# Kernel tuning notes

Hardware: AMD Instinct MI355X
Metric: run time of the kernel (lower is better)

Reference implementation:

```python
import jax, jax.numpy as jnp
import numpy as np

L = 6      # layers (enc and dec)
D = 512    # d_model
H = 8      # heads
DK = D // H
F = 2048   # dim_feedforward
B = 8
S = 512    # src len
T = 512    # tgt len
NEG = -1e9


def setup_inputs() -> dict:
    key = jax.random.key(0)
    ks = jax.random.split(key, 64)
    it = iter(ks)
    def w(shape, scale=0.02):
        return jax.random.normal(next(it), shape, dtype=jnp.float32) * scale
    inp = {}
    inp['src'] = jax.random.normal(next(it), (B, S, D), dtype=jnp.float32)
    inp['tgt'] = jax.random.normal(next(it), (B, T, D), dtype=jnp.float32)
    inp['tgt_mask'] = jnp.where(jnp.triu(jnp.ones((T, T), bool), 1), jnp.float32(NEG), jnp.float32(0.0))
    # encoder params (stacked over L layers)
    inp['enc_Wq'] = w((L, H, D, DK)); inp['enc_Wk'] = w((L, H, D, DK)); inp['enc_Wv'] = w((L, H, D, DK))
    inp['enc_Wo'] = w((L, D, D))
    inp['enc_ln1_a'] = jnp.ones((L, D)); inp['enc_ln1_b'] = jnp.zeros((L, D))
    inp['enc_W1'] = w((L, D, F)); inp['enc_b1'] = jnp.zeros((L, F))
    inp['enc_W2'] = w((L, F, D)); inp['enc_b2'] = jnp.zeros((L, D))
    inp['enc_ln2_a'] = jnp.ones((L, D)); inp['enc_ln2_b'] = jnp.zeros((L, D))
    # decoder params
    inp['dec_sWq'] = w((L, H, D, DK)); inp['dec_sWk'] = w((L, H, D, DK)); inp['dec_sWv'] = w((L, H, D, DK))
    inp['dec_sWo'] = w((L, D, D))
    inp['dec_ln1_a'] = jnp.ones((L, D)); inp['dec_ln1_b'] = jnp.zeros((L, D))
    inp['dec_cWq'] = w((L, H, D, DK)); inp['dec_cWk'] = w((L, H, D, DK)); inp['dec_cWv'] = w((L, H, D, DK))
    inp['dec_cWo'] = w((L, D, D))
    inp['dec_ln2_a'] = jnp.ones((L, D)); inp['dec_ln2_b'] = jnp.zeros((L, D))
    inp['dec_W1'] = w((L, D, F)); inp['dec_b1'] = jnp.zeros((L, F))
    inp['dec_W2'] = w((L, F, D)); inp['dec_b2'] = jnp.zeros((L, D))
    inp['dec_ln3_a'] = jnp.ones((L, D)); inp['dec_ln3_b'] = jnp.zeros((L, D))
    return inp


def layernorm(x, a, b):
    # faithful to the torch module: unbiased std (ddof=1) and eps added to std
    mean = x.mean(-1, keepdims=True)
    std = jnp.std(x, axis=-1, keepdims=True, ddof=1)
    return a * (x - mean) / (std + 1e-6) + b


def mha(qx, kx, vx, Wq, Wk, Wv, Wo, mask):
    # Wq/Wk/Wv: [H, D, dk] (per-head torch loop fused into one batched einsum)
    q = jnp.einsum('bsd,hdk->bhsk', qx, Wq)
    k = jnp.einsum('bsd,hdk->bhsk', kx, Wk)
    v = jnp.einsum('bsd,hdk->bhsk', vx, Wv)
    scores = jnp.einsum('bhqk,bhmk->bhqm', q, k) / np.float32(np.sqrt(Wq.shape[-1]))
    if mask is not None:
        scores = scores + mask  # [T,T] broadcasts over batch and heads
    attn = jax.nn.softmax(scores, axis=-1)
    o = jnp.einsum('bhqm,bhmk->bhqk', attn, v)
    b_, h_, s_, k_ = o.shape
    o = o.transpose(0, 2, 1, 3).reshape(b_, s_, h_ * k_)  # concat heads
    return o @ Wo


def ffn(x, W1, b1, W2, b2):
    return jnp.maximum(x @ W1 + b1, 0.0) @ W2 + b2


def reference(src, tgt, tgt_mask,
              enc_Wq, enc_Wk, enc_Wv, enc_Wo, enc_ln1_a, enc_ln1_b,
              enc_W1, enc_b1, enc_W2, enc_b2, enc_ln2_a, enc_ln2_b,
              dec_sWq, dec_sWk, dec_sWv, dec_sWo, dec_ln1_a, dec_ln1_b,
              dec_cWq, dec_cWk, dec_cWv, dec_cWo, dec_ln2_a, dec_ln2_b,
              dec_W1, dec_b1, dec_W2, dec_b2, dec_ln3_a, dec_ln3_b):
    # encoder
    x = src
    for i in range(L):
        h = x + mha(x, x, x, enc_Wq[i], enc_Wk[i], enc_Wv[i], enc_Wo[i], None)
        x = layernorm(h, enc_ln1_a[i], enc_ln1_b[i])
        h = x + ffn(x, enc_W1[i], enc_b1[i], enc_W2[i], enc_b2[i])
        x = layernorm(h, enc_ln2_a[i], enc_ln2_b[i])
    memory = x
    # decoder
    y = tgt
    for i in range(L):
        h = y + mha(y, y, y, dec_sWq[i], dec_sWk[i], dec_sWv[i], dec_sWo[i], tgt_mask)
        y = layernorm(h, dec_ln1_a[i], dec_ln1_b[i])
        h = y + mha(y, memory, memory, dec_cWq[i], dec_cWk[i], dec_cWv[i], dec_cWo[i], None)
        y = layernorm(h, dec_ln2_a[i], dec_ln2_b[i])
        h = y + ffn(y, dec_W1[i], dec_b1[i], dec_W2[i], dec_b2[i])
        y = layernorm(h, dec_ln3_a[i], dec_ln3_b[i])
    return y
```

## Files before the change

### kernel.cpp

```cpp
#include <hip/hip_runtime.h>
#include <hip/hip_bf16.h>

typedef unsigned short u16;
typedef __hip_bfloat16 hbf;
typedef __bf16 bf16x8 __attribute__((ext_vector_type(8)));
typedef float f32x4 __attribute__((ext_vector_type(4)));

#define LL 6
#define DD 512
#define HH 8
#define DKK 64
#define FF 2048
#define BB 8
#define SS 512

#define GLL(gp, lp)                                                        \
  __builtin_amdgcn_global_load_lds(                                        \
      (const __attribute__((address_space(1))) void*)(gp),                 \
      (__attribute__((address_space(3))) void*)(lp), 16, 0, 0)

__global__ __launch_bounds__(256) void cvt_k(const float* __restrict__ x,
                                             hbf* __restrict__ y, int n) {
  for (int i = (blockIdx.x * 256 + threadIdx.x) * 4; i < n; i += gridDim.x * 1024) {
    float4 v = *(const float4*)(x + i);
    y[i] = __float2bfloat16(v.x);
    y[i + 1] = __float2bfloat16(v.y);
    y[i + 2] = __float2bfloat16(v.z);
    y[i + 3] = __float2bfloat16(v.w);
  }
}

__global__ __launch_bounds__(256) void transpose_k(const float* __restrict__ src,
                                                   hbf* __restrict__ dst, int R, int C) {
  __shared__ hbf tile[64][65];
  const int b = blockIdx.z;
  src += (size_t)b * R * C;
  dst += (size_t)b * R * C;
  int c0 = blockIdx.x * 64, r0 = blockIdx.y * 64;
  int tx = threadIdx.x & 63;
  int ty = threadIdx.x >> 6;
#pragma unroll
  for (int i = 0; i < 16; i++) {
    int r = ty + i * 4;
    tile[r][tx] = __float2bfloat16(src[(size_t)(r0 + r) * C + c0 + tx]);
  }
  __syncthreads();
#pragma unroll
  for (int i = 0; i < 16; i++) {
    int r = ty + i * 4;
    dst[(size_t)(c0 + r) * R + r0 + tx] = tile[tx][r];
  }
}

__global__ __launch_bounds__(256) void transpose_qkv_k(const float* __restrict__ Wq,
                                                       const float* __restrict__ Wk,
                                                       const float* __restrict__ Wv,
                                                       hbf* __restrict__ dst) {
  __shared__ hbf tile[64][65];
  const int z = blockIdx.z;
  const int l = z / 24, r = z - l * 24;
  const int zw = r >> 3, h = r & 7;
  const float* src =
      (zw == 0 ? Wq : (zw == 1 ? Wk : Wv)) + ((size_t)l * HH + h) * DD * DKK;
  const int r0 = blockIdx.y * 64;
  const int tx = threadIdx.x & 63, ty = threadIdx.x >> 6;
#pragma unroll
  for (int i = 0; i < 16; i++) {
    int rr = ty + i * 4;
    tile[rr][tx] = __float2bfloat16(src[(size_t)(r0 + rr) * DKK + tx]);
  }
  __syncthreads();
  hbf* d = dst + (size_t)l * 3 * DD * DD + ((size_t)zw * 512 + h * 64) * DD + r0;
#pragma unroll
  for (int i = 0; i < 16; i++) {
    int rr = ty + i * 4;
    d[(size_t)rr * DD + tx] = tile[tx][rr];
  }
}

template <int BM, int MODE, int SPLITK>
__global__ __launch_bounds__(128) void gemm_nt(
    const u16* __restrict__ A, const u16* __restrict__ Bm, void* __restrict__ Cout,
    void* __restrict__ C2, void* __restrict__ C3,
    const float* __restrict__ bias, const hbf* __restrict__ res,
    int M, int N, int K, int lda, int ldb, int ldc, int ncoloff,
    long sAo, long sAi, long sBo, long sBi, long sCo, long sCi, int inner, float scale) {
  constexpr int BN = 64, BK = 64;
  constexpr int AM = BM / 32;
  constexpr int NCA = BM / 16;
  constexpr int WR = BM / 2;
  __shared__ u16 As[BM * BK];
  __shared__ u16 Bs[BN * BK];

  int bxx = blockIdx.x, byy = blockIdx.y;
  {
    const int gx = gridDim.x, gy = gridDim.y;
    const int f = byy * gx + bxx;
    const int st = gy >> 3;
    const int rem = f >> 3;
    byy = (f & 7) * st + rem % st;
    bxx = rem / st;
  }

  int g = blockIdx.z;
  int ks = 0;
  if (SPLITK > 1) {
    ks = g;
    g = 0;
  }
  int outer = g / inner, inr = g - outer * inner;
  A += outer * sAo + inr * sAi;
  Bm += outer * sBo + inr * sBi;

  const int tid = threadIdx.x;
  const int m0 = byy * BM, n0 = (bxx + ncoloff) * BN;
  const int wave = tid >> 6, lane = tid & 63;
  const int m16 = lane & 15, quad = lane >> 4;
  const int l8 = lane & 7, ld8 = lane >> 3;
  const int scol = (l8 ^ ld8) << 3;

  const u16* Ab = A + (size_t)m0 * lda;
  const u16* Bb = Bm + (size_t)n0 * ldb;

  f32x4 acc[AM][4] = {};

  const int kbeg = ks * (K / SPLITK), kend = kbeg + K / SPLITK;
  for (int k0 = kbeg; k0 < kend; k0 += BK) {
#pragma unroll
    for (int c = 0; c < NCA; c++) {
      const int ch = wave * NCA + c;
      const int row = ch * 8 + ld8;
      GLL(Ab + (size_t)row * lda + k0 + scol, &As[ch * 512]);
    }
#pragma unroll
    for (int c = 0; c < 4; c++) {
      const int ch = wave * 4 + c;
      const int row = ch * 8 + ld8;
      GLL(Bb + (size_t)row * ldb + k0 + scol, &Bs[ch * 512]);
    }
    __syncthreads();
#pragma unroll
    for (int kc = 0; kc < 2; kc++) {
      bf16x8 af[AM], bfv[4];
      const int sw = (((kc << 2) | quad) ^ (m16 & 7)) << 3;
#pragma unroll
      for (int i = 0; i < AM; i++)
        af[i] = *(const bf16x8*)(&As[(wave * WR + i * 16 + m16) * 64 + sw]);
#pragma unroll
      for (int j = 0; j < 4; j++)
        bfv[j] = *(const bf16x8*)(&Bs[(j * 16 + m16) * 64 + sw]);
#pragma unroll
      for (int i = 0; i < AM; i++)
#pragma unroll
        for (int j = 0; j < 4; j++)
          acc[i][j] = __builtin_amdgcn_mfma_f32_16x16x32_bf16(af[i], bfv[j], acc[i][j], 0, 0, 0);
    }
    __syncthreads();
  }

#pragma unroll
  for (int i = 0; i < AM; i++) {
#pragma unroll
    for (int j = 0; j < 4; j++) {
      const int col = n0 + j * 16 + m16;
      const int rowb = m0 + wave * WR + i * 16 + quad * 4;
#pragma unroll
      for (int r = 0; r < 4; r++) {
        const int row = rowb + r;
        float v = acc[i][j][r] * scale;
        if (MODE == 0) {
          hbf* C = (hbf*)Cout + outer * sCo + inr * sCi;
          C[(size_t)row * ldc + col] = __float2bfloat16(v);
        } else if (MODE == 2) {
          float* C = (float*)((SPLITK > 1 && ks == 1) ? C2 : Cout);
          C += outer * sCo + inr * sCi;
          if (SPLITK == 1 || ks == 0) {
            if (bias) v += bias[col];
            if (res) v += __bfloat162float(res[(size_t)row * ldc + col]);
          }
          C[(size_t)row * ldc + col] = v;
        } else if (MODE == 3) {
          hbf* C = (hbf*)Cout + outer * sCo + inr * sCi;
          v += bias[col];
          C[(size_t)row * ldc + col] = __float2bfloat16(fmaxf(v, 0.0f));
        } else if (MODE == 4) {
          const int b = row >> 9, s = row & 511;
          const int which = col >> 9, h = (col >> 6) & 7, dk = col & 63;
          const int bh = (b << 3) + h;
          if (which == 0)
            ((hbf*)Cout)[((size_t)bh * SS + s) * DKK + dk] = __float2bfloat16(v * 0.125f);
          else if (which == 1)
            ((hbf*)C2)[((size_t)bh * SS + s) * DKK + dk] = __float2bfloat16(v);
          else
            ((hbf*)C3)[((size_t)bh * DKK + dk) * SS + s] = __float2bfloat16(v);
        }
      }
    }
  }
}

__global__ __launch_bounds__(256) void flash_k(const u16* __restrict__ Q,
                                               const u16* __restrict__ Kb,
                                               const u16* __restrict__ Vt,
                                               hbf* __restrict__ O, int causal) {
  __shared__ u16 Qs[32][72];
  __shared__ u16 Ks[128 * 72];
  __shared__ u16 Ss[32][520];
  const int bh = blockIdx.y;
  const int q0 = blockIdx.x * 32;
  const int b = bh >> 3, h = bh & 7;
  const int tid = threadIdx.x;
  const int wave = tid >> 6, lane = tid & 63;
  const int m16 = lane & 15, quad = lane >> 4;
  const int rg = (wave >> 1) * 16;
  const int chf = wave & 1;

  const u16* Qp = Q + ((size_t)bh * SS + q0) * DKK;
  const u16* Kp = Kb + (size_t)bh * SS * DKK;
  const u16* Vp = Vt + (size_t)bh * DKK * SS;

  {
    int row = tid >> 3, ch = (tid & 7) << 3;
    *(float4*)(&Qs[row][ch]) = *(const float4*)(Qp + (size_t)row * DKK + ch);
  }

  for (int kt = 0; kt < 4; kt++) {
    if (kt > 0) __syncthreads();
#pragma unroll
    for (int p = 0; p < 4; p++) {
      int idx = p * 256 + tid;
      int row = idx >> 3, ch = (idx & 7) << 3;
      *(float4*)(&Ks[row * 72 + ch]) =
          *(const float4*)(Kp + (size_t)(kt * 128 + row) * DKK + ch);
    }
    __syncthreads();
#pragma unroll
    for (int ct = 0; ct < 4; ct++) {
      f32x4 s{};
#pragma unroll
      for (int kc = 0; kc < 2; kc++) {
        bf16x8 a = *(const bf16x8*)(&Qs[rg + m16][kc * 32 + quad * 8]);
        bf16x8 bv =
            *(const bf16x8*)(&Ks[(chf * 64 + ct * 16 + m16) * 72 + kc * 32 + quad * 8]);
        s = __builtin_amdgcn_mfma_f32_16x16x32_bf16(a, bv, s, 0, 0, 0);
      }
      const int colb = kt * 128 + chf * 64 + ct * 16 + m16;
#pragma unroll
      for (int r = 0; r < 4; r++)
        *((hbf*)&Ss[rg + quad * 4 + r][colb]) = __float2bfloat16(s[r]);
    }
  }
  __syncthreads();

#pragma unroll
  for (int rr = 0; rr < 8; rr++) {
    const int r = wave * 8 + rr;
    const int gr = q0 + r;
    float v[8];
#pragma unroll
    for (int i = 0; i < 8; i++) {
      const int col = lane + i * 64;
      v[i] = __bfloat162float(((const hbf*)Ss[r])[col]);
      if (causal && col > gr) v[i] = -1e30f;
    }
    float m = v[0];
#pragma unroll
    for (int i = 1; i < 8; i++) m = fmaxf(m, v[i]);
#pragma unroll
    for (int off = 1; off < 64; off <<= 1) m = fmaxf(m, __shfl_xor(m, off));
    float e[8], s = 0.f;
#pragma unroll
    for (int i = 0; i < 8; i++) {
      e[i] = __expf(v[i] - m);
      s += e[i];
    }
#pragma unroll
    for (int off = 1; off < 64; off <<= 1) s += __shfl_xor(s, off);
    const float inv = 1.0f / s;
#pragma unroll
    for (int i = 0; i < 8; i++)
      ((hbf*)Ss[r])[lane + i * 64] = __float2bfloat16(e[i] * inv);
  }
  __syncthreads();

  f32x4 o[2] = {};
  u16* Vs = Ks;
  for (int vt = 0; vt < 4; vt++) {
    if (vt > 0) __syncthreads();
#pragma unroll
    for (int p = 0; p < 4; p++) {
      int idx = p * 256 + tid;
      int row = idx >> 4, ch = (idx & 15) << 3;
      *(float4*)(&Vs[row * 136 + ch]) =
          *(const float4*)(Vp + (size_t)row * SS + vt * 128 + ch);
    }
    __syncthreads();
#pragma unroll
    for (int kc = 0; kc < 4; kc++) {
      bf16x8 a = *(const bf16x8*)(&Ss[rg + m16][vt * 128 + kc * 32 + quad * 8]);
#pragma unroll
      for (int dt = 0; dt < 2; dt++) {
        bf16x8 bv =
            *(const bf16x8*)(&Vs[(chf * 32 + dt * 16 + m16) * 136 + kc * 32 + quad * 8]);
        o[dt] = __builtin_amdgcn_mfma_f32_16x16x32_bf16(a, bv, o[dt], 0, 0, 0);
      }
    }
  }
#pragma unroll
  for (int dt = 0; dt < 2; dt++) {
    const int d = h * 64 + chf * 32 + dt * 16 + m16;
#pragma unroll
    for (int r = 0; r < 4; r++) {
      const int row = q0 + rg + quad * 4 + r;
      O[(size_t)b * SS * DD + (size_t)row * DD + d] = __float2bfloat16(o[dt][r]);
    }
  }
}

template <typename T>
__global__ __launch_bounds__(256) void layernorm_k(const float* __restrict__ X,
                                                   const float* __restrict__ X2,
                                                   const float* __restrict__ ga,
                                                   const float* __restrict__ gb,
                                                   T* __restrict__ out, int Dn) {
  const int row = blockIdx.x;
  X += (size_t)row * Dn;
  X2 += (size_t)row * Dn;
  out += (size_t)row * Dn;
  const int t = threadIdx.x;
  float2 xv = *(const float2*)(X + 2 * t);
  float2 x2 = *(const float2*)(X2 + 2 * t);
  xv.x += x2.x;
  xv.y += x2.y;
  float s = xv.x + xv.y, ss = xv.x * xv.x + xv.y * xv.y;
#pragma unroll
  for (int off = 32; off > 0; off >>= 1) {
    s += __shfl_down(s, off);
    ss += __shfl_down(ss, off);
  }
  __shared__ float sm[8];
  __shared__ float smean, sinv;
  const int wv = t >> 6, ln = t & 63;
  if (ln == 0) {
    sm[wv] = s;
    sm[4 + wv] = ss;
  }
  __syncthreads();
  if (t == 0) {
    float S1 = sm[0] + sm[1] + sm[2] + sm[3];
    float S2 = sm[4] + sm[5] + sm[6] + sm[7];
    float mean = S1 / Dn;
    float var = (S2 - S1 * mean) / (Dn - 1);
    var = fmaxf(var, 0.0f);
    smean = mean;
    sinv = 1.0f / (sqrtf(var) + 1e-6f);
  }
  __syncthreads();
  const float mean = smean, inv = sinv;
  float o0 = ga[2 * t] * (xv.x - mean) * inv + gb[2 * t];
  float o1 = ga[2 * t + 1] * (xv.y - mean) * inv + gb[2 * t + 1];
  if constexpr (sizeof(T) == 2) {
    out[2 * t] = (T)__float2bfloat16(o0);
    out[2 * t + 1] = (T)__float2bfloat16(o1);
  } else {
    out[2 * t] = o0;
    out[2 * t + 1] = o1;
  }
}

extern "C" void kernel_launch(void* const* d_in, const int* in_sizes, int n_in,
                              void* d_out, int out_size, void* d_ws, size_t ws_size,
                              hipStream_t stream) {
  (void)in_sizes; (void)n_in; (void)out_size;
  const float* src = (const float*)d_in[0];
  const float* tgt = (const float*)d_in[1];
  const float* eWq = (const float*)d_in[3];
  const float* eWk = (const float*)d_in[4];
  const float* eWv = (const float*)d_in[5];
  const float* eWo = (const float*)d_in[6];
  const float* eln1a = (const float*)d_in[7];
  const float* eln1b = (const float*)d_in[8];
  const float* eW1 = (const float*)d_in[9];
  const float* eb1 = (const float*)d_in[10];
  const float* eW2 = (const float*)d_in[11];
  const float* eb2 = (const float*)d_in[12];
  const float* eln2a = (const float*)d_in[13];
  const float* eln2b = (const float*)d_in[14];
  const float* sWq = (const float*)d_in[15];
  const float* sWk = (const float*)d_in[16];
  const float* sWv = (const float*)d_in[17];
  const float* sWo = (const float*)d_in[18];
  const float* dln1a = (const float*)d_in[19];
  const float* dln1b = (const float*)d_in[20];
  const float* cWq = (const float*)d_in[21];
  const float* cWk = (const float*)d_in[22];
  const float* cWv = (const float*)d_in[23];
  const float* cWo = (const float*)d_in[24];
  const float* dln2a = (const float*)d_in[25];
  const float* dln2b = (const float*)d_in[26];
  const float* dW1 = (const float*)d_in[27];
  const float* db1 = (const float*)d_in[28];
  const float* dW2 = (const float*)d_in[29];
  const float* db2 = (const float*)d_in[30];
  const float* dln3a = (const float*)d_in[31];
  const float* dln3b = (const float*)d_in[32];

  const size_t MB = 1024 * 1024;
  char* ws = (char*)d_ws;
  const size_t QKV_L = (size_t)3 * DD * DD;
  const size_t WO_L = (size_t)DD * DD;
  const size_t WF_L = (size_t)DD * FF;
  const bool preT = ws_size >= 150 * MB;

  hbf *qkvT_all = nullptr, *woT_all = nullptr, *w1T_all = nullptr, *w2T_all = nullptr;
  hbf *wqkvS = nullptr, *woS = nullptr, *w1S = nullptr, *w2S = nullptr;
  char* actb;
  if (preT) {
    qkvT_all = (hbf*)(ws);
    woT_all = (hbf*)(ws + 28311552);
    w1T_all = (hbf*)(ws + 37748736);
    w2T_all = (hbf*)(ws + 62914560);
    actb = ws + 84 * MB;
  } else {
    if (ws_size < 72 * MB) return;
    wqkvS = (hbf*)(ws);
    woS = (hbf*)(ws + 2 * MB);
    w1S = (hbf*)(ws + 2 * MB + 512 * 1024);
    w2S = (hbf*)(ws + 4 * MB + 512 * 1024);
    actb = ws + 7 * MB;
  }
  hbf* sbuf = (hbf*)(actb);
  u16* xbuf = (u16*)(actb + 4 * MB);
  hbf* tbuf = (hbf*)(actb + 8 * MB);
  u16* ybuf = (u16*)(actb + 12 * MB);
  u16* qbuf = (u16*)(actb + 16 * MB);
  u16* kbuf = (u16*)(actb + 20 * MB);
  u16* vtb = (u16*)(actb + 24 * MB);
  u16* obuf = (u16*)(actb + 28 * MB);
  u16* ffnh = (u16*)(actb + 32 * MB);
  float* projf = (float*)(actb + 48 * MB);
  float* projf2 = (float*)(actb + 56 * MB);

  const size_t WQL = (size_t)HH * DD * DKK;
  const size_t WOL = (size_t)DD * DD;
  const size_t WFL = (size_t)DD * FF;

  if (preT) {
    transpose_qkv_k<<<dim3(1, 8, LL * 24), dim3(256), 0, stream>>>(eWq, eWk, eWv, qkvT_all);
    transpose_qkv_k<<<dim3(1, 8, LL * 24), dim3(256), 0, stream>>>(sWq, sWk, sWv,
                                                                   qkvT_all + LL * QKV_L);
    transpose_qkv_k<<<dim3(1, 8, LL * 24), dim3(256), 0, stream>>>(
        cWq, cWk, cWv, qkvT_all + 2 * LL * QKV_L);
    transpose_k<<<dim3(8, 8, LL), dim3(256), 0, stream>>>(eWo, woT_all, DD, DD);
    transpose_k<<<dim3(8, 8, LL), dim3(256), 0, stream>>>(sWo, woT_all + LL * WO_L, DD, DD);
    transpose_k<<<dim3(8, 8, LL), dim3(256), 0, stream>>>(cWo, woT_all + 2 * LL * WO_L, DD, DD);
    transpose_k<<<dim3(32, 8, LL), dim3(256), 0, stream>>>(eW1, w1T_all, DD, FF);
    transpose_k<<<dim3(32, 8, LL), dim3(256), 0, stream>>>(dW1, w1T_all + LL * WF_L, DD, FF);
    transpose_k<<<dim3(8, 32, LL), dim3(256), 0, stream>>>(eW2, w2T_all, FF, DD);
    transpose_k<<<dim3(8, 32, LL), dim3(256), 0, stream>>>(dW2, w2T_all + LL * WF_L, FF, DD);
  }

  auto attention = [&](const u16* qin, const u16* kvin, const hbf* qkvTl, const hbf* woTl,
                       const u16* resid, int causal) {
    if (qin == kvin) {
      gemm_nt<128, 4, 1><<<dim3(24, 32, 1), dim3(128), 0, stream>>>(
          qin, (const u16*)qkvTl, qbuf, kbuf, vtb, nullptr, nullptr, BB * SS, 3 * DD, DD,
          DD, DD, 0, 0, 0, 0, 0, 0, 0, 0, 1, 1.f);
    } else {
      gemm_nt<64, 4, 1><<<dim3(8, 64, 1), dim3(128), 0, stream>>>(
          qin, (const u16*)qkvTl, qbuf, kbuf, vtb, nullptr, nullptr, BB * SS, DD, DD,
          DD, DD, 0, 0, 0, 0, 0, 0, 0, 0, 1, 1.f);
      gemm_nt<64, 4, 1><<<dim3(16, 64, 1), dim3(128), 0, stream>>>(
          kvin, (const u16*)qkvTl, qbuf, kbuf, vtb, nullptr, nullptr, BB * SS, 3 * DD, DD,
          DD, DD, 0, 8, 0, 0, 0, 0, 0, 0, 1, 1.f);
    }
    flash_k<<<dim3(16, 64), dim3(256), 0, stream>>>(qbuf, kbuf, vtb, (hbf*)obuf, causal);
    gemm_nt<64, 2, 2><<<dim3(8, 64, 2), dim3(128), 0, stream>>>(
        obuf, (const u16*)woTl, projf, projf2, nullptr, nullptr, (const hbf*)resid,
        BB * SS, DD, DD, DD, DD, DD, 0, 0, 0, 0, 0, 0, 0, 1, 1.f);
  };

  auto ffn = [&](const u16* xin, const hbf* w1Tl, const float* b1l, const hbf* w2Tl,
                 const float* b2l) {
    gemm_nt<128, 3, 1><<<dim3(32, 32, 1), dim3(128), 0, stream>>>(
        xin, (const u16*)w1Tl, ffnh, nullptr, nullptr, b1l, nullptr, BB * SS, FF, DD,
        DD, DD, FF, 0, 0, 0, 0, 0, 0, 0, 1, 1.f);
    gemm_nt<64, 2, 2><<<dim3(8, 64, 2), dim3(128), 0, stream>>>(
        ffnh, (const u16*)w2Tl, projf, projf2, nullptr, b2l, (const hbf*)xin, BB * SS, DD,
        FF, FF, FF, DD, 0, 0, 0, 0, 0, 0, 0, 1, 1.f);
  };

  auto lnb = [&](const float* X, const float* a, const float* b, u16* out) {
    layernorm_k<hbf><<<dim3(BB * SS), dim3(256), 0, stream>>>(X, projf2, a, b, (hbf*)out, DD);
  };

  cvt_k<<<dim3(2048), dim3(256), 0, stream>>>(src, sbuf, BB * SS * DD);
  cvt_k<<<dim3(2048), dim3(256), 0, stream>>>(tgt, tbuf, BB * SS * DD);

  const u16* cur = (const u16*)sbuf;
  for (int l = 0; l < LL; l++) {
    const hbf *qkvTl, *woTl, *w1Tl, *w2Tl;
    if (preT) {
      qkvTl = qkvT_all + (size_t)l * QKV_L;
      woTl = woT_all + (size_t)l * WO_L;
      w1Tl = w1T_all + (size_t)l * WF_L;
      w2Tl = w2T_all + (size_t)l * WF_L;
    } else {
      transpose_qkv_k<<<dim3(1, 8, 24), dim3(256), 0, stream>>>(
          eWq + l * WQL, eWk + l * WQL, eWv + l * WQL, wqkvS);
      transpose_k<<<dim3(8, 8, 1), dim3(256), 0, stream>>>(eWo + l * WOL, woS, DD, DD);
      qkvTl = wqkvS;
      woTl = woS;
    }
    attention(cur, cur, qkvTl, woTl, cur, 0);
    lnb(projf, eln1a + l * DD, eln1b + l * DD, xbuf);
    if (!preT) {
      transpose_k<<<dim3(32, 8, 1), dim3(256), 0, stream>>>(eW1 + l * WFL, w1S, DD, FF);
      transpose_k<<<dim3(8, 32, 1), dim3(256), 0, stream>>>(eW2 + l * WFL, w2S, FF, DD);
      w1Tl = w1S;
      w2Tl = w2S;
    }
    ffn(xbuf, w1Tl, eb1 + l * FF, w2Tl, eb2 + l * DD);
    lnb(projf, eln2a + l * DD, eln2b + l * DD, xbuf);
    cur = xbuf;
  }
  const u16* mem = cur;
  const u16* yc = (const u16*)tbuf;
  for (int l = 0; l < LL; l++) {
    const hbf *sqkvTl, *swoTl, *cqkvTl, *cwoTl, *w1Tl, *w2Tl;
    if (preT) {
      sqkvTl = qkvT_all + ((size_t)LL + l) * QKV_L;
      swoTl = woT_all + ((size_t)LL + l) * WO_L;
      cqkvTl = qkvT_all + ((size_t)2 * LL + l) * QKV_L;
      cwoTl = woT_all + ((size_t)2 * LL + l) * WO_L;
      w1Tl = w1T_all + ((size_t)LL + l) * WF_L;
      w2Tl = w2T_all + ((size_t)LL + l) * WF_L;
    }
    if (!preT) {
      transpose_qkv_k<<<dim3(1, 8, 24), dim3(256), 0, stream>>>(
          sWq + l * WQL, sWk + l * WQL, sWv + l * WQL, wqkvS);
      transpose_k<<<dim3(8, 8, 1), dim3(256), 0, stream>>>(sWo + l * WOL, woS, DD, DD);
      sqkvTl = wqkvS;
      swoTl = woS;
    }
    attention(yc, yc, sqkvTl, swoTl, yc, 1);
    lnb(projf, dln1a + l * DD, dln1b + l * DD, ybuf);
    yc = ybuf;
    if (!preT) {
      transpose_qkv_k<<<dim3(1, 8, 24), dim3(256), 0, stream>>>(
          cWq + l * WQL, cWk + l * WQL, cWv + l * WQL, wqkvS);
      transpose_k<<<dim3(8, 8, 1), dim3(256), 0, stream>>>(cWo + l * WOL, woS, DD, DD);
      cqkvTl = wqkvS;
      cwoTl = woS;
    }
    attention(yc, mem, cqkvTl, cwoTl, yc, 0);
    lnb(projf, dln2a + l * DD, dln2b + l * DD, ybuf);
    if (!preT) {
      transpose_k<<<dim3(32, 8, 1), dim3(256), 0, stream>>>(dW1 + l * WFL, w1S, DD, FF);
      transpose_k<<<dim3(8, 32, 1), dim3(256), 0, stream>>>(dW2 + l * WFL, w2S, FF, DD);
      w1Tl = w1S;
      w2Tl = w2S;
    }
    ffn(ybuf, w1Tl, db1 + l * FF, w2Tl, db2 + l * DD);
    if (l == LL - 1) {
      layernorm_k<float><<<dim3(BB * SS), dim3(256), 0, stream>>>(
          projf, projf2, dln3a + l * DD, dln3b + l * DD, (float*)d_out, DD);
    } else {
      lnb(projf, dln3a + l * DD, dln3b + l * DD, ybuf);
      yc = ybuf;
    }
  }
}
```

Measured before the change: 2.113 ms.

## Double-buffer GEMM tiles, skip masked causal key tiles, fuse cross-attn QKV launch

Measured after the change: 2.112 ms. Within noise of the previous version (-0.1%).

```diff
diff --git a/kernel.cpp b/kernel.cpp
--- a/kernel.cpp
+++ b/kernel.cpp
@@ -84,13 +84,14 @@
     void* __restrict__ C2, void* __restrict__ C3,
     const float* __restrict__ bias, const hbf* __restrict__ res,
     int M, int N, int K, int lda, int ldb, int ldc, int ncoloff,
-    long sAo, long sAi, long sBo, long sBi, long sCo, long sCi, int inner, float scale) {
+    long sAo, long sAi, long sBo, long sBi, long sCo, long sCi, int inner, float scale,
+    const u16* __restrict__ A2) {
   constexpr int BN = 64, BK = 64;
   constexpr int AM = BM / 32;
   constexpr int NCA = BM / 16;
   constexpr int WR = BM / 2;
-  __shared__ u16 As[BM * BK];
-  __shared__ u16 Bs[BN * BK];
+  __shared__ u16 As[2][BM * BK];
+  __shared__ u16 Bs[2][BN * BK];
 
   int bxx = blockIdx.x, byy = blockIdx.y;
   {
@@ -119,36 +120,45 @@
   const int l8 = lane & 7, ld8 = lane >> 3;
   const int scol = (l8 ^ ld8) << 3;
 
-  const u16* Ab = A + (size_t)m0 * lda;
+  const u16* Asel = (MODE == 4 && n0 >= 512) ? A2 : A;
+  const u16* Ab = Asel + (size_t)m0 * lda;
   const u16* Bb = Bm + (size_t)n0 * ldb;
 
   f32x4 acc[AM][4] = {};
 
-  const int kbeg = ks * (K / SPLITK), kend = kbeg + K / SPLITK;
-  for (int k0 = kbeg; k0 < kend; k0 += BK) {
+  const int kbeg = ks * (K / SPLITK);
+  const int nt = (K / SPLITK) / BK;
+
+  auto stage = [&](int b, int k0) {
 #pragma unroll
     for (int c = 0; c < NCA; c++) {
       const int ch = wave * NCA + c;
       const int row = ch * 8 + ld8;
-      GLL(Ab + (size_t)row * lda + k0 + scol, &As[ch * 512]);
+      GLL(Ab + (size_t)row * lda + k0 + scol, &As[b][ch * 512]);
     }
 #pragma unroll
     for (int c = 0; c < 4; c++) {
       const int ch = wave * 4 + c;
       const int row = ch * 8 + ld8;
-      GLL(Bb + (size_t)row * ldb + k0 + scol, &Bs[ch * 512]);
-    }
-    __syncthreads();
+      GLL(Bb + (size_t)row * ldb + k0 + scol, &Bs[b][ch * 512]);
+    }
+  };
+
+  stage(0, kbeg);
+  __syncthreads();
+  for (int t = 0; t < nt; t++) {
+    if (t + 1 < nt) stage((t + 1) & 1, kbeg + (t + 1) * BK);
+    const int cb = t & 1;
 #pragma unroll
     for (int kc = 0; kc < 2; kc++) {
       bf16x8 af[AM], bfv[4];
       const int sw = (((kc << 2) | quad) ^ (m16 & 7)) << 3;
 #pragma unroll
       for (int i = 0; i < AM; i++)
-        af[i] = *(const bf16x8*)(&As[(wave * WR + i * 16 + m16) * 64 + sw]);
+        af[i] = *(const bf16x8*)(&As[cb][(wave * WR + i * 16 + m16) * 64 + sw]);
 #pragma unroll
       for (int j = 0; j < 4; j++)
-        bfv[j] = *(const bf16x8*)(&Bs[(j * 16 + m16) * 64 + sw]);
+        bfv[j] = *(const bf16x8*)(&Bs[cb][(j * 16 + m16) * 64 + sw]);
 #pragma unroll
       for (int i = 0; i < AM; i++)
 #pragma unroll
@@ -219,12 +229,14 @@
   const u16* Kp = Kb + (size_t)bh * SS * DKK;
   const u16* Vp = Vt + (size_t)bh * DKK * SS;
 
+  const int ktmax = causal ? ((q0 + 31) >> 7) + 1 : 4;
+
   {
     int row = tid >> 3, ch = (tid & 7) << 3;
     *(float4*)(&Qs[row][ch]) = *(const float4*)(Qp + (size_t)row * DKK + ch);
   }
 
-  for (int kt = 0; kt < 4; kt++) {
+  for (int kt = 0; kt < ktmax; kt++) {
     if (kt > 0) __syncthreads();
 #pragma unroll
     for (int p = 0; p < 4; p++) {
@@ -285,7 +297,7 @@
 
   f32x4 o[2] = {};
   u16* Vs = Ks;
-  for (int vt = 0; vt < 4; vt++) {
+  for (int vt = 0; vt < ktmax; vt++) {
     if (vt > 0) __syncthreads();
 #pragma unroll
     for (int p = 0; p < 4; p++) {
@@ -462,32 +474,27 @@
 
   auto attention = [&](const u16* qin, const u16* kvin, const hbf* qkvTl, const hbf* woTl,
                        const u16* resid, int causal) {
-    if (qin == kvin) {
-      gemm_nt<128, 4, 1><<<dim3(24, 32, 1), dim3(128), 0, stream>>>(
-          qin, (const u16*)qkvTl, qbuf, kbuf, vtb, nullptr, nullptr, BB * SS, 3 * DD, DD,
-          DD, DD, 0, 0, 0, 0, 0, 0, 0, 0, 1, 1.f);
-    } else {
-      gemm_nt<64, 4, 1><<<dim3(8, 64, 1), dim3(128), 0, stream>>>(
-          qin, (const u16*)qkvTl, qbuf, kbuf, vtb, nullptr, nullptr, BB * SS, DD, DD,
-          DD, DD, 0, 0, 0, 0, 0, 0, 0, 0, 1, 1.f);
-      gemm_nt<64, 4, 1><<<dim3(16, 64, 1), dim3(128), 0, stream>>>(
-          kvin, (const u16*)qkvTl, qbuf, kbuf, vtb, nullptr, nullptr, BB * SS, 3 * DD, DD,
-          DD, DD, 0, 8, 0, 0, 0, 0, 0, 0, 1, 1.f);
-    }
+    gemm_nt<128, 4, 1><<<dim3(24, 32, 1), dim3(128), 0, stream>>>(
+        qin, (const u16*)qkvTl, qbuf, kbuf, vtb, nullptr, nullptr,
+        BB * SS, 3 * DD, DD, DD, DD, 0, 0,
+        0, 0, 0, 0, 0, 0, 1, 1.f, kvin);
     flash_k<<<dim3(16, 64), dim3(256), 0, stream>>>(qbuf, kbuf, vtb, (hbf*)obuf, causal);
     gemm_nt<64, 2, 2><<<dim3(8, 64, 2), dim3(128), 0, stream>>>(
         obuf, (const u16*)woTl, projf, projf2, nullptr, nullptr, (const hbf*)resid,
-        BB * SS, DD, DD, DD, DD, DD, 0, 0, 0, 0, 0, 0, 0, 1, 1.f);
+        BB * SS, DD, DD, DD, DD, DD, 0,
+        0, 0, 0, 0, 0, 0, 1, 1.f, nullptr);
   };
 
   auto ffn = [&](const u16* xin, const hbf* w1Tl, const float* b1l, const hbf* w2Tl,
                  const float* b2l) {
     gemm_nt<128, 3, 1><<<dim3(32, 32, 1), dim3(128), 0, stream>>>(
-        xin, (const u16*)w1Tl, ffnh, nullptr, nullptr, b1l, nullptr, BB * SS, FF, DD,
-        DD, DD, FF, 0, 0, 0, 0, 0, 0, 0, 1, 1.f);
+        xin, (const u16*)w1Tl, ffnh, nullptr, nullptr, b1l, nullptr,
+        BB * SS, FF, DD, DD, DD, FF, 0,
+        0, 0, 0, 0, 0, 0, 1, 1.f, nullptr);
     gemm_nt<64, 2, 2><<<dim3(8, 64, 2), dim3(128), 0, stream>>>(
-        ffnh, (const u16*)w2Tl, projf, projf2, nullptr, b2l, (const hbf*)xin, BB * SS, DD,
-        FF, FF, FF, DD, 0, 0, 0, 0, 0, 0, 0, 1, 1.f);
+        ffnh, (const u16*)w2Tl, projf, projf2, nullptr, b2l, (const hbf*)xin,
+        BB * SS, DD, FF, FF, FF, DD, 0,
+        0, 0, 0, 0, 0, 0, 1, 1.f, nullptr);
   };
 
   auto lnb = [&](const float* X, const float* a, const float* b, u16* out) {
```
